# Kernel optimization log

Measured on AMD Instinct MI355X. Metric: run time of the kernel, lower is better.

## Reference

```python
import jax, jax.numpy as jnp
import numpy as np

B, N, C, H = 64, 1024, 512, 8
D = C // H            # head dim = 64
WIN = 32
M = 64                # num_landmarks
HP, WP = 8, 8         # closest_square_factors(64)
ITERS = 6
SCALE = D ** -0.5


def activ(x):
    # ExpLinearAfterThreshold with max_val=0: exp(clamp(x, max=0)) + relu(x)
    return jnp.exp(jnp.minimum(x, 0.0)) + jax.nn.relu(x)


def moore_penrose_iter_pinv(x, iters=ITERS):
    abs_x = jnp.abs(x)
    denom = jnp.max(abs_x.sum(axis=-1)) * jnp.max(abs_x.sum(axis=-2))
    z = jnp.swapaxes(x, -1, -2) / denom
    I = jnp.eye(x.shape[-1], dtype=x.dtype)
    for _ in range(iters):
        xz = x @ z
        z = 0.25 * z @ (13.0 * I - xz @ (15.0 * I - xz @ (7.0 * I - xz)))
    return z


def pool_landmarks(t):
    t = t.reshape(B, H, HP, WIN // HP, WP, WIN // WP, D)
    return t.mean(axis=(3, 5)).reshape(B, H, M, D)


def setup_inputs() -> dict:
    key = jax.random.key(0)
    ks = jax.random.split(key, 7)
    s = 0.02
    x = jax.random.normal(ks[0], (B, N, C), jnp.float32)
    Wq = jax.random.normal(ks[1], (C, C), jnp.float32) * s
    bq = jnp.zeros((C,), jnp.float32)
    Wkv = jax.random.normal(ks[2], (C, 2 * C), jnp.float32) * s
    bkv = jnp.zeros((2 * C,), jnp.float32)
    Wp = jax.random.normal(ks[3], (C, C), jnp.float32) * s
    bp = jnp.zeros((C,), jnp.float32)
    return {"x": x, "Wq": Wq, "bq": bq, "Wkv": Wkv, "bkv": bkv, "Wp": Wp, "bp": bp}


def reference(x, Wq, bq, Wkv, bkv, Wp, bp):
    Bsz = x.shape[0]
    q = (x @ Wq + bq).reshape(Bsz, N, H, D).transpose(0, 2, 1, 3) * SCALE  # [B,H,N,D]
    kv = (x @ Wkv + bkv).reshape(Bsz, N, 2, H, D).transpose(2, 0, 3, 1, 4)
    k, v = kv[0], kv[1]                                                    # [B,H,N,D]

    q_m = pool_landmarks(q)   # [B,H,M,D]
    k_m = pool_landmarks(k)   # [B,H,M,D]

    temp = activ(jnp.einsum('bhmd,bhnd->bhmn', q_m, k_m))   # [B,H,M,M]
    pinv = moore_penrose_iter_pinv(temp, ITERS)

    v1 = jnp.concatenate([v, jnp.ones_like(v[..., :1])], axis=-1)          # [B,H,N,D+1]
    kern_qkm = activ(jnp.einsum('bhnd,bhmd->bhnm', q, k_m))                # [B,H,N,M]
    kern_qmk_v = activ(jnp.einsum('bhmd,bhnd->bhmn', q_m, k)) @ v1         # [B,H,M,D+1]

    prod = kern_qkm @ (pinv @ kern_qmk_v)                                  # [B,H,N,D+1]
    out = prod[..., :-1] / (prod[..., -1:] + 1e-12)                        # [B,H,N,D]
    out = out.transpose(0, 2, 1, 3).reshape(Bsz, N, C)
    return out @ Wp + bp
```

## Files before the change

### kernel.cpp

```cpp
#include <hip/hip_runtime.h>

typedef _Float16 f16;
typedef _Float16 f16x4 __attribute__((ext_vector_type(4)));
typedef _Float16 f16x8 __attribute__((ext_vector_type(8)));
typedef float f32x4 __attribute__((ext_vector_type(4)));

#define MFMA16(a, b, c) __builtin_amdgcn_mfma_f32_16x16x32_f16((a), (b), (c), 0, 0, 0)

__device__ __forceinline__ void gload16(const void* g, void* l) {
  __builtin_amdgcn_global_load_lds(
      (const __attribute__((address_space(1))) void*)g,
      (__attribute__((address_space(3))) void*)l, 16, 0, 0);
}

__device__ __forceinline__ f16x8 lds8(const f16* buf, int row, int ch) {
  return *(const f16x8*)(buf + row * 64 + ((ch ^ (row & 7)) << 3));
}

#define VMW8 asm volatile("s_waitcnt vmcnt(8)" ::: "memory")
#define VMW0 asm volatile("s_waitcnt vmcnt(0)" ::: "memory")
#define BAR __builtin_amdgcn_s_barrier()


__global__ __launch_bounds__(256) void k_prep_w(
    const float* __restrict__ Wq, const float* __restrict__ Wkv,
    const float* __restrict__ Wp, const float* __restrict__ bq,
    const float* __restrict__ bkv, f16* __restrict__ WcT,
    f16* __restrict__ WpT, float* __restrict__ bc) {
  int b = blockIdx.x, t = threadIdx.x;
  if (b < 1536) {
    for (int kk = t; kk < 512; kk += 256) {
      float w = (b < 512) ? Wq[kk * 512 + b] : Wkv[kk * 1024 + (b - 512)];
      WcT[b * 512 + kk] = (f16)w;
    }
    if (t == 0) bc[b] = (b < 512) ? bq[b] : bkv[b - 512];
  } else {
    int pc = b - 1536;
    for (int kk = t; kk < 512; kk += 256)
      WpT[pc * 512 + kk] = (f16)Wp[kk * 512 + pc];
  }
}

__global__ __launch_bounds__(256) void k_prep_x(const float* __restrict__ x,
                                                f16* __restrict__ xh,
                                                float* __restrict__ xm) {
  __shared__ float pl[4][8][512];
  int bid = blockIdx.x;
  int b = bid >> 3, a = bid & 7;
  int tid = threadIdx.x;
  int tr = tid >> 6, cl = tid & 63;
  int c0 = cl * 8;
  float pacc[8][8];
#pragma unroll
  for (int i = 0; i < 8; i++)
#pragma unroll
    for (int j = 0; j < 8; j++) pacc[i][j] = 0.f;
#pragma unroll
  for (int j = 0; j < 32; j++) {
    int n = a * 128 + tr * 32 + j;
    const float* row = x + (size_t)(b * 1024 + n) * 512 + c0;
    float4 v0 = *(const float4*)row;
    float4 v1 = *(const float4*)(row + 4);
    f16x8 h;
    h[0] = (f16)v0.x; h[1] = (f16)v0.y; h[2] = (f16)v0.z; h[3] = (f16)v0.w;
    h[4] = (f16)v1.x; h[5] = (f16)v1.y; h[6] = (f16)v1.z; h[7] = (f16)v1.w;
    *(f16x8*)(xh + (size_t)(b * 1024 + n) * 512 + c0) = h;
    int cg = j >> 2;
    pacc[cg][0] += v0.x; pacc[cg][1] += v0.y; pacc[cg][2] += v0.z;
    pacc[cg][3] += v0.w; pacc[cg][4] += v1.x; pacc[cg][5] += v1.y;
    pacc[cg][6] += v1.z; pacc[cg][7] += v1.w;
  }
#pragma unroll
  for (int cg = 0; cg < 8; cg++) {
    *(float4*)&pl[tr][cg][c0] =
        make_float4(pacc[cg][0], pacc[cg][1], pacc[cg][2], pacc[cg][3]);
    *(float4*)&pl[tr][cg][c0 + 4] =
        make_float4(pacc[cg][4], pacc[cg][5], pacc[cg][6], pacc[cg][7]);
  }
  __syncthreads();
#pragma unroll
  for (int s = 0; s < 4; s++) {
    int o = tid + s * 256;
    int cg = o >> 7, c4 = (o & 127) << 2;
    float4 r0 = *(const float4*)&pl[0][cg][c4];
    float4 r1 = *(const float4*)&pl[1][cg][c4];
    float4 r2 = *(const float4*)&pl[2][cg][c4];
    float4 r3 = *(const float4*)&pl[3][cg][c4];
    float4 r;
    r.x = (r0.x + r1.x + r2.x + r3.x) * 0.0625f;
    r.y = (r0.y + r1.y + r2.y + r3.y) * 0.0625f;
    r.z = (r0.z + r1.z + r2.z + r3.z) * 0.0625f;
    r.w = (r0.w + r1.w + r2.w + r3.w) * 0.0625f;
    *(float4*)(xm + (size_t)(b * 64 + a * 8 + cg) * 512 + c4) = r;
  }
}

__global__ __launch_bounds__(512) void k_qkv(
    const f16* __restrict__ xh, const f16* __restrict__ WcT,
    const float* __restrict__ bc, f16* __restrict__ qb, f16* __restrict__ kb,
    f16* __restrict__ vb) {
  __shared__ f16 Al[2][256 * 64];
  __shared__ f16 Bl[2][256 * 64];
  int bid = blockIdx.x;
  int swz = (bid & 7) * 192 + (bid >> 3);
  int ct = swz % 6, rt = swz / 6;
  int m0 = rt * 256, n0 = ct * 256;
  int tid = threadIdx.x, lane = tid & 63, w = tid >> 6;
  int lr = lane & 15, hi = lane >> 4;
  int wr = w >> 2, wc = w & 3;

  int srow = tid >> 3;
  int cg = (tid & 7) ^ (srow & 7);
  const f16* gA = xh + (size_t)(m0 + srow) * 512 + cg * 8;
  const f16* gB = WcT + (size_t)(n0 + srow) * 512 + cg * 8;

  f32x4 acc[4][8] = {};

#define STG(BUF, K0)                                                \
  {                                                                 \
    _Pragma("unroll") for (int s = 0; s < 4; s++) {                 \
      gload16(gA + (K0) + s * 64 * 512, &Al[BUF][tid * 8 + s * 4096]); \
      gload16(gB + (K0) + s * 64 * 512, &Bl[BUF][tid * 8 + s * 4096]); \
    }                                                               \
  }
#define CMP(BUF)                                                    \
  {                                                                 \
    __builtin_amdgcn_s_setprio(1);                                  \
    _Pragma("unroll") for (int kc = 0; kc < 2; kc++) {              \
      f16x8 af[4], bf[8];                                           \
      _Pragma("unroll") for (int ni = 0; ni < 4; ni++)              \
          af[ni] = lds8(&Bl[BUF][0], wc * 64 + ni * 16 + lr, kc * 4 + hi); \
      _Pragma("unroll") for (int mi = 0; mi < 8; mi++)              \
          bf[mi] = lds8(&Al[BUF][0], wr * 128 + mi * 16 + lr, kc * 4 + hi); \
      _Pragma("unroll") for (int ni = 0; ni < 4; ni++)              \
          _Pragma("unroll") for (int mi = 0; mi < 8; mi++)          \
              acc[ni][mi] = MFMA16(af[ni], bf[mi], acc[ni][mi]);    \
    }                                                               \
    __builtin_amdgcn_s_setprio(0);                                  \
  }

  STG(0, 0);
  STG(1, 64);
  VMW8; BAR; CMP(0); BAR; STG(0, 2 * 64);
  VMW8; BAR; CMP(1); BAR; STG(1, 3 * 64);
  VMW8; BAR; CMP(0); BAR; STG(0, 4 * 64);
  VMW8; BAR; CMP(1); BAR; STG(1, 5 * 64);
  VMW8; BAR; CMP(0); BAR; STG(0, 6 * 64);
  VMW8; BAR; CMP(1); BAR; STG(1, 7 * 64);
  VMW8; BAR; CMP(0);
  VMW0; BAR; CMP(1);
#undef STG
#undef CMP

  int region = n0 >> 9;
  f16* dst = region == 0 ? qb : (region == 1 ? kb : vb);
  float scale = region == 0 ? 0.125f : 1.0f;
  int ncol0 = n0 - region * 512;
  float4 bias[4];
#pragma unroll
  for (int ni = 0; ni < 4; ni++)
    bias[ni] = *(const float4*)(bc + region * 512 + ncol0 + wc * 64 + ni * 16 +
                                hi * 4);
#pragma unroll
  for (int mi = 0; mi < 8; mi++) {
    int gr = m0 + wr * 128 + mi * 16 + lr;
    int b = gr >> 10, n = gr & 1023;
#pragma unroll
    for (int ni = 0; ni < 4; ni++) {
      int cc = ncol0 + wc * 64 + ni * 16 + hi * 4;
      int h = cc >> 6, d = cc & 63;
      f16x4 hv;
      hv[0] = (f16)((acc[ni][mi][0] + bias[ni].x) * scale);
      hv[1] = (f16)((acc[ni][mi][1] + bias[ni].y) * scale);
      hv[2] = (f16)((acc[ni][mi][2] + bias[ni].z) * scale);
      hv[3] = (f16)((acc[ni][mi][3] + bias[ni].w) * scale);
      *(f16x4*)(dst + (size_t)(((b * 8 + h) * 1024 + n) * 64 + d)) = hv;
    }
  }
}

__global__ __launch_bounds__(512) void k_qmkm(
    const float* __restrict__ xm, const float* __restrict__ Wq,
    const float* __restrict__ Wkv, const float* __restrict__ bq,
    const float* __restrict__ bkv, float* __restrict__ qm,
    float* __restrict__ km) {
  __shared__ float xl[16][512];
  int bid = blockIdx.x;
  int b = bid >> 2, mg = bid & 3;
  int tid = threadIdx.x;
  for (int s = 0; s < 4; s++) {
    int idx = (tid + s * 512) * 4;
    int r = idx >> 9, cc = idx & 511;
    *(float4*)&xl[r][cc] =
        *(const float4*)(xm + (b * 64 + mg * 16 + r) * 512 + cc);
  }
  __syncthreads();
  int oc = tid;
  float aq[16] = {}, ak[16] = {};
  for (int cc = 0; cc < 512; cc += 4) {
    float wq0 = Wq[(cc + 0) * 512 + oc], wq1 = Wq[(cc + 1) * 512 + oc];
    float wq2 = Wq[(cc + 2) * 512 + oc], wq3 = Wq[(cc + 3) * 512 + oc];
    float wk0 = Wkv[(cc + 0) * 1024 + oc], wk1 = Wkv[(cc + 1) * 1024 + oc];
    float wk2 = Wkv[(cc + 2) * 1024 + oc], wk3 = Wkv[(cc + 3) * 1024 + oc];
    for (int mi = 0; mi < 16; mi++) {
      float4 xv = *(const float4*)&xl[mi][cc];
      aq[mi] += xv.x * wq0 + xv.y * wq1 + xv.z * wq2 + xv.w * wq3;
      ak[mi] += xv.x * wk0 + xv.y * wk1 + xv.z * wk2 + xv.w * wk3;
    }
  }
  int h = oc >> 6, d = oc & 63;
  for (int mi = 0; mi < 16; mi++) {
    int m = mg * 16 + mi;
    int base = ((b * 8 + h) * 64 + m) * 64 + d;
    qm[base] = (aq[mi] + bq[oc]) * 0.125f;
    km[base] = ak[mi] + bkv[oc];
  }
}

__global__ __launch_bounds__(256) void k_temp(const float* __restrict__ qm,
                                              const float* __restrict__ km,
                                              float* __restrict__ temp,
                                              unsigned* __restrict__ den) {
  __shared__ float ql[64][68], kl[64][68];
  __shared__ float rs[64], cs[64];
  int g = blockIdx.x, tid = threadIdx.x;
  for (int idx = tid; idx < 4096; idx += 256) {
    int r = idx >> 6, c = idx & 63;
    ql[r][c] = qm[g * 4096 + idx];
    kl[r][c] = km[g * 4096 + idx];
  }
  __syncthreads();
  int ti = tid >> 4, tj = tid & 15;
  float acc[4][4] = {};
  for (int kk = 0; kk < 64; kk += 4) {
    float4 qa[4], kb[4];
    for (int i = 0; i < 4; i++) qa[i] = *(const float4*)&ql[ti * 4 + i][kk];
    for (int j = 0; j < 4; j++) kb[j] = *(const float4*)&kl[tj * 4 + j][kk];
    for (int i = 0; i < 4; i++)
      for (int j = 0; j < 4; j++)
        acc[i][j] += qa[i].x * kb[j].x + qa[i].y * kb[j].y +
                     qa[i].z * kb[j].z + qa[i].w * kb[j].w;
  }
  float e[4][4];
  for (int i = 0; i < 4; i++)
    for (int j = 0; j < 4; j++) {
      float xx = acc[i][j];
      e[i][j] = xx > 0.f ? 1.f + xx : __expf(xx);
    }
  __syncthreads();
  for (int i = 0; i < 4; i++)
    for (int j = 0; j < 4; j++) kl[ti * 4 + i][tj * 4 + j] = e[i][j];
  __syncthreads();
  for (int idx = tid; idx < 4096; idx += 256)
    temp[g * 4096 + idx] = kl[idx >> 6][idx & 63];
  if (tid < 64) {
    float s = 0.f;
    for (int j = 0; j < 64; j++) s += kl[tid][j];
    rs[tid] = s;
  } else if (tid < 128) {
    int c = tid - 64;
    float s = 0.f;
    for (int i = 0; i < 64; i++) s += kl[i][c];
    cs[c] = s;
  }
  __syncthreads();
  if (tid == 0) {
    float mx = rs[0];
    for (int i = 1; i < 64; i++) mx = fmaxf(mx, rs[i]);
    atomicMax(den + 0, __float_as_uint(mx));
  }
  if (tid == 1) {
    float mx = cs[0];
    for (int i = 1; i < 64; i++) mx = fmaxf(mx, cs[i]);
    atomicMax(den + 1, __float_as_uint(mx));
  }
}

__global__ __launch_bounds__(256) void k_pinv(const float* __restrict__ temp,
                                              const unsigned* __restrict__ den,
                                              float* __restrict__ z) {
  __shared__ f16 wh[64][72], Zh[64][72], ZhT[64][72], GhT[64][72], W1h[64][72],
      W2h[64][72];
  __shared__ float colZ[64];
  int g = blockIdx.x, tid = threadIdx.x;
  float dn = __uint_as_float(den[0]) * __uint_as_float(den[1]);
  float inv = 1.0f / dn;
  for (int idx = tid; idx < 4096; idx += 256) {
    int r = idx >> 6, c = idx & 63;
    float t = temp[g * 4096 + idx];
    wh[r][c] = (f16)(t - 1.0f);
    ZhT[r][c] = (f16)(t * inv);
  }
  __syncthreads();
  for (int idx = tid; idx < 4096; idx += 256) {
    int r = idx >> 6, c = idx & 63;
    Zh[r][c] = ZhT[c][r];
  }
  __syncthreads();
  int lane = tid & 63, w = tid >> 6, lr = lane & 15, hi = lane >> 4;
  int rb = w * 16;
  for (int it = 0; it < 6; it++) {
    if (tid < 64) {
      float s = 0.f;
      for (int i = 0; i < 64; i++) s += (float)ZhT[tid][i];
      colZ[tid] = s;
    }
    __syncthreads();
    {
      f32x4 acc[4] = {};
      for (int kc = 0; kc < 2; kc++) {
        f16x8 a = *(const f16x8*)&wh[rb + lr][kc * 32 + hi * 8];
        for (int cj = 0; cj < 4; cj++)
          acc[cj] = MFMA16(
              a, *(const f16x8*)&ZhT[cj * 16 + lr][kc * 32 + hi * 8], acc[cj]);
      }
      for (int cj = 0; cj < 4; cj++)
        for (int rg = 0; rg < 4; rg++) {
          int rr = rb + hi * 4 + rg, cc = cj * 16 + lr;
          GhT[cc][rr] = (f16)(acc[cj][rg] + colZ[cc]);
        }
    }
    __syncthreads();
    {
      f32x4 acc[4] = {};
      for (int kc = 0; kc < 2; kc++) {
        f16x8 a = *(const f16x8*)&Zh[rb + lr][kc * 32 + hi * 8];
        for (int cj = 0; cj < 4; cj++)
          acc[cj] = MFMA16(
              a, *(const f16x8*)&GhT[cj * 16 + lr][kc * 32 + hi * 8], acc[cj]);
      }
      for (int cj = 0; cj < 4; cj++)
        for (int rg = 0; rg < 4; rg++)
          W1h[rb + hi * 4 + rg][cj * 16 + lr] = (f16)acc[cj][rg];
    }
    __syncthreads();
    {
      f32x4 acc[4] = {};
      for (int kc = 0; kc < 2; kc++) {
        f16x8 a = *(const f16x8*)&W1h[rb + lr][kc * 32 + hi * 8];
        for (int cj = 0; cj < 4; cj++)
          acc[cj] = MFMA16(
              a, *(const f16x8*)&GhT[cj * 16 + lr][kc * 32 + hi * 8], acc[cj]);
      }
      for (int cj = 0; cj < 4; cj++)
        for (int rg = 0; rg < 4; rg++)
          W2h[rb + hi * 4 + rg][cj * 16 + lr] = (f16)acc[cj][rg];
    }
    __syncthreads();
    {
      f32x4 acc[4] = {};
      for (int kc = 0; kc < 2; kc++) {
        f16x8 a = *(const f16x8*)&W2h[rb + lr][kc * 32 + hi * 8];
        for (int cj = 0; cj < 4; cj++)
          acc[cj] = MFMA16(
              a, *(const f16x8*)&GhT[cj * 16 + lr][kc * 32 + hi * 8], acc[cj]);
      }
      for (int cj = 0; cj < 4; cj++)
        for (int rg = 0; rg < 4; rg++) {
          int rr = rb + hi * 4 + rg, cc = cj * 16 + lr;
          float zn = 3.25f * (float)Zh[rr][cc] - 3.75f * (float)W1h[rr][cc] +
                     1.75f * (float)W2h[rr][cc] - 0.25f * acc[cj][rg];
          if (it == 5) {
            z[g * 4096 + rr * 64 + cc] = zn;
          } else {
            Zh[rr][cc] = (f16)zn;
            ZhT[cc][rr] = (f16)zn;
          }
        }
    }
    __syncthreads();
  }
}

__global__ __launch_bounds__(256) void k_kqmkv(const float* __restrict__ qm,
                                               const f16* __restrict__ kb,
                                               const f16* __restrict__ vb,
                                               float* __restrict__ kq) {
  __shared__ f16 qh[64][72];
  __shared__ f16 Sl[64][136];
  __shared__ f16 vt[80][136];
  int g = blockIdx.x, tid = threadIdx.x;
  int lane = tid & 63, w = tid >> 6, lr = lane & 15, hi = lane >> 4;
  for (int idx = tid; idx < 4096; idx += 256) {
    int r = idx >> 6, c = idx & 63;
    qh[r][c] = (f16)qm[g * 4096 + idx];
  }
  for (int idx = tid; idx < 16 * 136; idx += 256) {
    int r = 64 + idx / 136, c = idx % 136;
    vt[r][c] = (r == 64) ? (f16)1.0f : (f16)0.0f;
  }
  f32x4 acc2[5] = {};
  const f16* kbase = kb + g * 65536;
  const f16* vbase = vb + g * 65536;
  for (int n0 = 0; n0 < 1024; n0 += 128) {
    __syncthreads();
    for (int s = 0; s < 4; s++) {
      int cid = tid + s * 256;
      int r = cid >> 3, ch = cid & 7;
      f16x8 v8 = *(const f16x8*)(vbase + (n0 + r) * 64 + ch * 8);
      for (int j = 0; j < 8; j++) vt[ch * 8 + j][r] = v8[j];
    }
    __syncthreads();
    f32x4 sacc[8] = {};
    for (int kc = 0; kc < 2; kc++) {
      f16x8 a = *(const f16x8*)&qh[w * 16 + lr][kc * 32 + hi * 8];
      for (int cj = 0; cj < 8; cj++) {
        f16x8 bv =
            *(const f16x8*)(kbase + (n0 + cj * 16 + lr) * 64 + kc * 32 + hi * 8);
        sacc[cj] = MFMA16(a, bv, sacc[cj]);
      }
    }
    for (int cj = 0; cj < 8; cj++)
      for (int rg = 0; rg < 4; rg++) {
        float xx = sacc[cj][rg];
        float e = xx > 0.f ? 1.f + xx : __expf(xx);
        Sl[w * 16 + hi * 4 + rg][cj * 16 + lr] = (f16)e;
      }
    __syncthreads();
    for (int kc2 = 0; kc2 < 4; kc2++) {
      f16x8 a = *(const f16x8*)&Sl[w * 16 + lr][kc2 * 32 + hi * 8];
      for (int ce = 0; ce < 5; ce++)
        acc2[ce] = MFMA16(
            a, *(const f16x8*)&vt[ce * 16 + lr][kc2 * 32 + hi * 8], acc2[ce]);
    }
  }
  for (int ce = 0; ce < 5; ce++)
    for (int rg = 0; rg < 4; rg++)
      kq[g * 5120 + (w * 16 + hi * 4 + rg) * 80 + ce * 16 + lr] = acc2[ce][rg];
}

__global__ __launch_bounds__(256) void k_w2(const float* __restrict__ z,
                                            const float* __restrict__ kq,
                                            f16* __restrict__ w2t) {
  __shared__ float zl[64][68];
  __shared__ float kl[64][84];
  int g = blockIdx.x, tid = threadIdx.x;
  for (int idx = tid; idx < 4096; idx += 256)
    zl[idx >> 6][idx & 63] = z[g * 4096 + idx];
  for (int idx = tid; idx < 5120; idx += 256)
    kl[idx / 80][idx % 80] = kq[g * 5120 + idx];
  __syncthreads();
  int ti = tid >> 4, tj = tid & 15;
  float acc[4][5] = {};
  for (int kk = 0; kk < 64; kk++) {
    float a0 = zl[ti * 4 + 0][kk], a1 = zl[ti * 4 + 1][kk];
    float a2 = zl[ti * 4 + 2][kk], a3 = zl[ti * 4 + 3][kk];
    for (int j = 0; j < 5; j++) {
      float bv = kl[kk][tj * 5 + j];
      acc[0][j] += a0 * bv; acc[1][j] += a1 * bv;
      acc[2][j] += a2 * bv; acc[3][j] += a3 * bv;
    }
  }
  for (int i = 0; i < 4; i++)
    for (int j = 0; j < 5; j++)
      w2t[g * 5120 + (tj * 5 + j) * 64 + (ti * 4 + i)] = (f16)acc[i][j];
}

__global__ __launch_bounds__(256) void k_attn(const f16* __restrict__ qb,
                                              const float* __restrict__ km,
                                              const f16* __restrict__ w2t,
                                              f16* __restrict__ attn) {
  __shared__ f16 kmh[64][72];
  __shared__ f16 w2l[80][72];
  __shared__ f16 Sl[128][72];
  int g = blockIdx.x;
  int b = g >> 3, h = g & 7;
  int tid = threadIdx.x, lane = tid & 63, w = tid >> 6, lr = lane & 15,
      hi = lane >> 4;
  for (int idx = tid; idx < 4096; idx += 256)
    kmh[idx >> 6][idx & 63] = (f16)km[g * 4096 + idx];
  for (int idx = tid; idx < 5120; idx += 256)
    w2l[idx >> 6][idx & 63] = w2t[g * 5120 + idx];
  __syncthreads();
  for (int nt = 0; nt < 8; nt++) {
    int n0 = nt * 128;
    if (nt) __syncthreads();
    const f16* qbase = qb + g * 65536 + n0 * 64;
    f32x4 sacc[2][4] = {};
    for (int kc = 0; kc < 2; kc++)
      for (int ri = 0; ri < 2; ri++) {
        f16x8 a = *(const f16x8*)(qbase + (w * 32 + ri * 16 + lr) * 64 +
                                  kc * 32 + hi * 8);
        for (int cj = 0; cj < 4; cj++)
          sacc[ri][cj] = MFMA16(
              a, *(const f16x8*)&kmh[cj * 16 + lr][kc * 32 + hi * 8],
              sacc[ri][cj]);
      }
    for (int ri = 0; ri < 2; ri++)
      for (int cj = 0; cj < 4; cj++)
        for (int rg = 0; rg < 4; rg++) {
          float xx = sacc[ri][cj][rg];
          Sl[w * 32 + ri * 16 + hi * 4 + rg][cj * 16 + lr] =
              (f16)(xx > 0.f ? 1.f + xx : __expf(xx));
        }
    __syncthreads();
    f32x4 accP[5][2] = {};
    for (int kc = 0; kc < 2; kc++)
      for (int ri = 0; ri < 2; ri++) {
        f16x8 bfrag =
            *(const f16x8*)&Sl[w * 32 + ri * 16 + lr][kc * 32 + hi * 8];
        for (int ce = 0; ce < 5; ce++)
          accP[ce][ri] = MFMA16(
              *(const f16x8*)&w2l[ce * 16 + lr][kc * 32 + hi * 8], bfrag,
              accP[ce][ri]);
      }
    for (int ri = 0; ri < 2; ri++) {
      float dv = __shfl(accP[4][ri][0], lr, 64);
      float rd = 1.0f / (dv + 1e-12f);
      int n = w * 32 + ri * 16 + lr;
      for (int ce = 0; ce < 4; ce++) {
        f16x4 hv;
        hv[0] = (f16)(accP[ce][ri][0] * rd);
        hv[1] = (f16)(accP[ce][ri][1] * rd);
        hv[2] = (f16)(accP[ce][ri][2] * rd);
        hv[3] = (f16)(accP[ce][ri][3] * rd);
        *(f16x4*)(attn + (size_t)(b * 1024 + n0 + n) * 512 + h * 64 +
                  ce * 16 + hi * 4) = hv;
      }
    }
  }
}

__global__ __launch_bounds__(512) void k_out(const f16* __restrict__ ah,
                                             const f16* __restrict__ WpT,
                                             const float* __restrict__ bp,
                                             float* __restrict__ out) {
  __shared__ f16 Al[2][256 * 64];
  __shared__ f16 Bl[2][256 * 64];
  int bid = blockIdx.x;
  int swz = (bid & 7) * 64 + (bid >> 3);
  int ct = swz & 1, rt = swz >> 1;
  int m0 = rt * 256, n0 = ct * 256;
  int tid = threadIdx.x, lane = tid & 63, w = tid >> 6;
  int lr = lane & 15, hi = lane >> 4;
  int wr = w >> 2, wc = w & 3;

  int srow = tid >> 3;
  int cg = (tid & 7) ^ (srow & 7);
  const f16* gA = ah + (size_t)(m0 + srow) * 512 + cg * 8;
  const f16* gB = WpT + (size_t)(n0 + srow) * 512 + cg * 8;

  f32x4 acc[4][8] = {};

#define STG(BUF, K0)                                                \
  {                                                                 \
    _Pragma("unroll") for (int s = 0; s < 4; s++) {                 \
      gload16(gA + (K0) + s * 64 * 512, &Al[BUF][tid * 8 + s * 4096]); \
      gload16(gB + (K0) + s * 64 * 512, &Bl[BUF][tid * 8 + s * 4096]); \
    }                                                               \
  }
#define CMP(BUF)                                                    \
  {                                                                 \
    __builtin_amdgcn_s_setprio(1);                                  \
    _Pragma("unroll") for (int kc = 0; kc < 2; kc++) {              \
      f16x8 af[4], bf[8];                                           \
      _Pragma("unroll") for (int ni = 0; ni < 4; ni++)              \
          af[ni] = lds8(&Bl[BUF][0], wc * 64 + ni * 16 + lr, kc * 4 + hi); \
      _Pragma("unroll") for (int mi = 0; mi < 8; mi++)              \
          bf[mi] = lds8(&Al[BUF][0], wr * 128 + mi * 16 + lr, kc * 4 + hi); \
      _Pragma("unroll") for (int ni = 0; ni < 4; ni++)              \
          _Pragma("unroll") for (int mi = 0; mi < 8; mi++)          \
              acc[ni][mi] = MFMA16(af[ni], bf[mi], acc[ni][mi]);    \
    }                                                               \
    __builtin_amdgcn_s_setprio(0);                                  \
  }

  STG(0, 0);
  STG(1, 64);
  VMW8; BAR; CMP(0); BAR; STG(0, 2 * 64);
  VMW8; BAR; CMP(1); BAR; STG(1, 3 * 64);
  VMW8; BAR; CMP(0); BAR; STG(0, 4 * 64);
  VMW8; BAR; CMP(1); BAR; STG(1, 5 * 64);
  VMW8; BAR; CMP(0); BAR; STG(0, 6 * 64);
  VMW8; BAR; CMP(1); BAR; STG(1, 7 * 64);
  VMW8; BAR; CMP(0);
  VMW0; BAR; CMP(1);
#undef STG
#undef CMP

  float4 bias[4];
#pragma unroll
  for (int ni = 0; ni < 4; ni++)
    bias[ni] = *(const float4*)(bp + n0 + wc * 64 + ni * 16 + hi * 4);
#pragma unroll
  for (int mi = 0; mi < 8; mi++) {
    int gr = m0 + wr * 128 + mi * 16 + lr;
#pragma unroll
    for (int ni = 0; ni < 4; ni++) {
      int gc = n0 + wc * 64 + ni * 16 + hi * 4;
      float4 v;
      v.x = acc[ni][mi][0] + bias[ni].x;
      v.y = acc[ni][mi][1] + bias[ni].y;
      v.z = acc[ni][mi][2] + bias[ni].z;
      v.w = acc[ni][mi][3] + bias[ni].w;
      *(float4*)(out + (size_t)gr * 512 + gc) = v;
    }
  }
}

extern "C" void kernel_launch(void* const* d_in, const int* in_sizes, int n_in,
                              void* d_out, int out_size, void* d_ws,
                              size_t ws_size, hipStream_t stream) {
  (void)in_sizes; (void)n_in; (void)out_size; (void)ws_size;
  const float* x = (const float*)d_in[0];
  const float* Wq = (const float*)d_in[1];
  const float* bq = (const float*)d_in[2];
  const float* Wkv = (const float*)d_in[3];
  const float* bkv = (const float*)d_in[4];
  const float* Wp = (const float*)d_in[5];
  const float* bp = (const float*)d_in[6];
  float* outp = (float*)d_out;

  char* ws = (char*)d_ws;
  size_t o = 0;
  auto take = [&](size_t bytes) {
    char* p = ws + o;
    o += (bytes + 255) & ~(size_t)255;
    return p;
  };
  f16* WcT = (f16*)take(1536 * 512 * 2);
  f16* WpT = (f16*)take(512 * 512 * 2);
  float* bc = (float*)take(1536 * 4);
  f16* xh = (f16*)take(67108864);
  f16* qb = (f16*)take(67108864);
  f16* kb = (f16*)take(67108864);
  f16* vb = (f16*)take(67108864);

  char* od = (char*)d_out;
  size_t s = 0;
  auto sub = [&](size_t bytes) {
    char* p = od + s;
    s += (bytes + 255) & ~(size_t)255;
    return p;
  };
  float* xm = (float*)sub(64 * 64 * 512 * 4);
  float* qm = (float*)sub(512 * 4096 * 4);
  float* km = (float*)sub(512 * 4096 * 4);
  float* temp = (float*)sub(512 * 4096 * 4);
  float* zz = (float*)sub(512 * 4096 * 4);
  float* kq = (float*)sub(512 * 64 * 80 * 4);
  f16* w2t = (f16*)sub(512 * 80 * 64 * 2);
  unsigned* den = (unsigned*)sub(256);
  f16* attn = vb;

  hipLaunchKernelGGL(k_prep_w, dim3(2048), dim3(256), 0, stream, Wq, Wkv, Wp,
                     bq, bkv, WcT, WpT, bc);
  hipLaunchKernelGGL(k_prep_x, dim3(512), dim3(256), 0, stream, x, xh, xm);
  hipLaunchKernelGGL(k_qkv, dim3(1536), dim3(512), 0, stream, xh, WcT, bc,
                     qb, kb, vb);
  hipLaunchKernelGGL(k_qmkm, dim3(256), dim3(512), 0, stream, xm, Wq, Wkv, bq,
                     bkv, qm, km);
  hipMemsetAsync(den, 0, 8, stream);
  hipLaunchKernelGGL(k_temp, dim3(512), dim3(256), 0, stream, qm, km, temp,
                     den);
  hipLaunchKernelGGL(k_pinv, dim3(512), dim3(256), 0, stream, temp, den, zz);
  hipLaunchKernelGGL(k_kqmkv, dim3(512), dim3(256), 0, stream, qm, kb, vb, kq);
  hipLaunchKernelGGL(k_w2, dim3(512), dim3(256), 0, stream, zz, kq, w2t);
  hipLaunchKernelGGL(k_attn, dim3(512), dim3(256), 0, stream, qb, km, w2t,
                     attn);
  hipLaunchKernelGGL(k_out, dim3(512), dim3(512), 0, stream, attn, WpT, bp,
                     outp);
}
```

Baseline: 572.0 us.

## Interleave global-to-LDS prefetch with MFMA phases in QKV and projection GEMMs

Replaces the coarse double-buffered stage/compute loop in both large GEMM kernels with a finer schedule. Each K-tile is split into four phases, and each phase issues two prefetch loads for the next tile before its MFMAs run. Fragments are loaded per phase, and barriers plus a scheduling fence separate LDS reads from the MFMA block. The aim is to hide global load latency behind compute and spread out memory issue, at the cost of more barriers per tile and tighter wait counts.

```diff
diff --git a/kernel.cpp b/kernel.cpp
--- a/kernel.cpp
+++ b/kernel.cpp
@@ -17,8 +17,9 @@
   return *(const f16x8*)(buf + row * 64 + ((ch ^ (row & 7)) << 3));
 }
 
-#define VMW8 asm volatile("s_waitcnt vmcnt(8)" ::: "memory")
 #define VMW0 asm volatile("s_waitcnt vmcnt(0)" ::: "memory")
+#define VMW2 asm volatile("s_waitcnt vmcnt(2)" ::: "memory")
+#define VMW4 asm volatile("s_waitcnt vmcnt(4)" ::: "memory")
 #define BAR __builtin_amdgcn_s_barrier()
 
 
@@ -95,6 +96,40 @@
   }
 }
 
+#define SA(BUF, K0, S) gload16(gA + (K0) + (S)*64*512, &Al[BUF][tid*8 + (S)*4096]);
+#define SB(BUF, K0, S) gload16(gB + (K0) + (S)*64*512, &Bl[BUF][tid*8 + (S)*4096]);
+#define PHASE(P, Q, ...)                                                  \
+  {                                                                       \
+    f16x8 af[4], bf[4];                                                   \
+    _Pragma("unroll") for (int ni = 0; ni < 4; ni++)                      \
+      af[ni] = lds8(&Bl[P][0], wc*64 + ni*16 + lr, ((Q)&1)*4 + hi);       \
+    _Pragma("unroll") for (int mj = 0; mj < 4; mj++)                      \
+      bf[mj] = lds8(&Al[P][0], wr*128 + (((Q)>>1)*4+mj)*16 + lr, ((Q)&1)*4 + hi); \
+    __VA_ARGS__                                                           \
+    BAR;                                                                  \
+    asm volatile("s_waitcnt lgkmcnt(0)" ::: "memory");                    \
+    __builtin_amdgcn_sched_barrier(0);                                    \
+    __builtin_amdgcn_s_setprio(1);                                        \
+    _Pragma("unroll") for (int ni = 0; ni < 4; ni++)                      \
+      _Pragma("unroll") for (int mj = 0; mj < 4; mj++)                    \
+        acc[ni][((Q)>>1)*4+mj] = MFMA16(af[ni], bf[mj], acc[ni][((Q)>>1)*4+mj]); \
+    __builtin_amdgcn_s_setprio(0);                                        \
+    BAR;                                                                  \
+  }
+#define GROUP(T)                                                          \
+  VMW2; BAR;                                                              \
+  PHASE((T)&1, 0, SB(1-((T)&1), ((T)+1)*64, 0) SB(1-((T)&1), ((T)+1)*64, 1)) \
+  PHASE((T)&1, 1, SB(1-((T)&1), ((T)+1)*64, 2) SB(1-((T)&1), ((T)+1)*64, 3)) \
+  VMW4; BAR;                                                              \
+  PHASE((T)&1, 2, SA(1-((T)&1), ((T)+1)*64, 0) SA(1-((T)&1), ((T)+1)*64, 2)) \
+  PHASE((T)&1, 3, SA(1-((T)&1), ((T)+1)*64, 1) SA(1-((T)&1), ((T)+1)*64, 3))
+#define GROUP_LAST(T)                                                     \
+  VMW0; BAR;                                                              \
+  PHASE((T)&1, 0, ) PHASE((T)&1, 1, ) PHASE((T)&1, 2, ) PHASE((T)&1, 3, )
+#define PROLOGUE                                                          \
+  SB(0, 0, 0) SB(0, 0, 1) SB(0, 0, 2) SB(0, 0, 3)                         \
+  SA(0, 0, 0) SA(0, 0, 2) SA(0, 0, 1) SA(0, 0, 3)
+
 __global__ __launch_bounds__(512) void k_qkv(
     const f16* __restrict__ xh, const f16* __restrict__ WcT,
     const float* __restrict__ bc, f16* __restrict__ qb, f16* __restrict__ kb,
@@ -116,41 +151,9 @@
 
   f32x4 acc[4][8] = {};
 
-#define STG(BUF, K0)                                                \
-  {                                                                 \
-    _Pragma("unroll") for (int s = 0; s < 4; s++) {                 \
-      gload16(gA + (K0) + s * 64 * 512, &Al[BUF][tid * 8 + s * 4096]); \
-      gload16(gB + (K0) + s * 64 * 512, &Bl[BUF][tid * 8 + s * 4096]); \
-    }                                                               \
-  }
-#define CMP(BUF)                                                    \
-  {                                                                 \
-    __builtin_amdgcn_s_setprio(1);                                  \
-    _Pragma("unroll") for (int kc = 0; kc < 2; kc++) {              \
-      f16x8 af[4], bf[8];                                           \
-      _Pragma("unroll") for (int ni = 0; ni < 4; ni++)              \
-          af[ni] = lds8(&Bl[BUF][0], wc * 64 + ni * 16 + lr, kc * 4 + hi); \
-      _Pragma("unroll") for (int mi = 0; mi < 8; mi++)              \
-          bf[mi] = lds8(&Al[BUF][0], wr * 128 + mi * 16 + lr, kc * 4 + hi); \
-      _Pragma("unroll") for (int ni = 0; ni < 4; ni++)              \
-          _Pragma("unroll") for (int mi = 0; mi < 8; mi++)          \
-              acc[ni][mi] = MFMA16(af[ni], bf[mi], acc[ni][mi]);    \
-    }                                                               \
-    __builtin_amdgcn_s_setprio(0);                                  \
-  }
-
-  STG(0, 0);
-  STG(1, 64);
-  VMW8; BAR; CMP(0); BAR; STG(0, 2 * 64);
-  VMW8; BAR; CMP(1); BAR; STG(1, 3 * 64);
-  VMW8; BAR; CMP(0); BAR; STG(0, 4 * 64);
-  VMW8; BAR; CMP(1); BAR; STG(1, 5 * 64);
-  VMW8; BAR; CMP(0); BAR; STG(0, 6 * 64);
-  VMW8; BAR; CMP(1); BAR; STG(1, 7 * 64);
-  VMW8; BAR; CMP(0);
-  VMW0; BAR; CMP(1);
-#undef STG
-#undef CMP
+  PROLOGUE
+  GROUP(0) GROUP(1) GROUP(2) GROUP(3) GROUP(4) GROUP(5) GROUP(6)
+  GROUP_LAST(7)
 
   int region = n0 >> 9;
   f16* dst = region == 0 ? qb : (region == 1 ? kb : vb);
@@ -542,41 +545,9 @@
 
   f32x4 acc[4][8] = {};
 
-#define STG(BUF, K0)                                                \
-  {                                                                 \
-    _Pragma("unroll") for (int s = 0; s < 4; s++) {                 \
-      gload16(gA + (K0) + s * 64 * 512, &Al[BUF][tid * 8 + s * 4096]); \
-      gload16(gB + (K0) + s * 64 * 512, &Bl[BUF][tid * 8 + s * 4096]); \
-    }                                                               \
-  }
-#define CMP(BUF)                                                    \
-  {                                                                 \
-    __builtin_amdgcn_s_setprio(1);                                  \
-    _Pragma("unroll") for (int kc = 0; kc < 2; kc++) {              \
-      f16x8 af[4], bf[8];                                           \
-      _Pragma("unroll") for (int ni = 0; ni < 4; ni++)              \
-          af[ni] = lds8(&Bl[BUF][0], wc * 64 + ni * 16 + lr, kc * 4 + hi); \
-      _Pragma("unroll") for (int mi = 0; mi < 8; mi++)              \
-          bf[mi] = lds8(&Al[BUF][0], wr * 128 + mi * 16 + lr, kc * 4 + hi); \
-      _Pragma("unroll") for (int ni = 0; ni < 4; ni++)              \
-          _Pragma("unroll") for (int mi = 0; mi < 8; mi++)          \
-              acc[ni][mi] = MFMA16(af[ni], bf[mi], acc[ni][mi]);    \
-    }                                                               \
-    __builtin_amdgcn_s_setprio(0);                                  \
-  }
-
-  STG(0, 0);
-  STG(1, 64);
-  VMW8; BAR; CMP(0); BAR; STG(0, 2 * 64);
-  VMW8; BAR; CMP(1); BAR; STG(1, 3 * 64);
-  VMW8; BAR; CMP(0); BAR; STG(0, 4 * 64);
-  VMW8; BAR; CMP(1); BAR; STG(1, 5 * 64);
-  VMW8; BAR; CMP(0); BAR; STG(0, 6 * 64);
-  VMW8; BAR; CMP(1); BAR; STG(1, 7 * 64);
-  VMW8; BAR; CMP(0);
-  VMW0; BAR; CMP(1);
-#undef STG
-#undef CMP
+  PROLOGUE
+  GROUP(0) GROUP(1) GROUP(2) GROUP(3) GROUP(4) GROUP(5) GROUP(6)
+  GROUP_LAST(7)
 
   float4 bias[4];
 #pragma unroll
```

Measured after the change: 593.7 us. 1.04x slower.

## Merge prep kernels, fold memset, shrink GEMM tiles to 128x128 with 256 threads

Applied to the files above, without the earlier changes.

Combines the weight-prep and x-prep kernels into one launch and zeroes the denominator counters inside it, so the separate memset and one kernel launch go away. The QKV and output-projection GEMMs move from 256x256 tiles with 512 threads to 128x128 tiles with 256 threads. This quadruples the block count and halves LDS use per block, which is meant to improve occupancy and load balance across CUs. The cost is lower per-block data reuse and more global and L2 traffic for the operand tiles.

```diff
diff --git a/kernel.cpp b/kernel.cpp
--- a/kernel.cpp
+++ b/kernel.cpp
@@ -22,32 +22,33 @@
 #define BAR __builtin_amdgcn_s_barrier()
 
 
-__global__ __launch_bounds__(256) void k_prep_w(
-    const float* __restrict__ Wq, const float* __restrict__ Wkv,
-    const float* __restrict__ Wp, const float* __restrict__ bq,
-    const float* __restrict__ bkv, f16* __restrict__ WcT,
-    f16* __restrict__ WpT, float* __restrict__ bc) {
-  int b = blockIdx.x, t = threadIdx.x;
-  if (b < 1536) {
-    for (int kk = t; kk < 512; kk += 256) {
-      float w = (b < 512) ? Wq[kk * 512 + b] : Wkv[kk * 1024 + (b - 512)];
-      WcT[b * 512 + kk] = (f16)w;
-    }
-    if (t == 0) bc[b] = (b < 512) ? bq[b] : bkv[b - 512];
-  } else {
-    int pc = b - 1536;
-    for (int kk = t; kk < 512; kk += 256)
-      WpT[pc * 512 + kk] = (f16)Wp[kk * 512 + pc];
-  }
-}
-
-__global__ __launch_bounds__(256) void k_prep_x(const float* __restrict__ x,
-                                                f16* __restrict__ xh,
-                                                float* __restrict__ xm) {
+__global__ __launch_bounds__(256) void k_prep(
+    const float* __restrict__ x, const float* __restrict__ Wq,
+    const float* __restrict__ Wkv, const float* __restrict__ Wp,
+    const float* __restrict__ bq, const float* __restrict__ bkv,
+    f16* __restrict__ xh, float* __restrict__ xm, f16* __restrict__ WcT,
+    f16* __restrict__ WpT, float* __restrict__ bc,
+    unsigned* __restrict__ den) {
   __shared__ float pl[4][8][512];
   int bid = blockIdx.x;
+  int tid = threadIdx.x;
+  if (bid >= 512) {
+    int b = bid - 512;
+    if (b < 1536) {
+      for (int kk = tid; kk < 512; kk += 256) {
+        float w = (b < 512) ? Wq[kk * 512 + b] : Wkv[kk * 1024 + (b - 512)];
+        WcT[b * 512 + kk] = (f16)w;
+      }
+      if (tid == 0) bc[b] = (b < 512) ? bq[b] : bkv[b - 512];
+      if (b == 0 && tid == 1) { den[0] = 0u; den[1] = 0u; }
+    } else {
+      int pc = b - 1536;
+      for (int kk = tid; kk < 512; kk += 256)
+        WpT[pc * 512 + kk] = (f16)Wp[kk * 512 + pc];
+    }
+    return;
+  }
   int b = bid >> 3, a = bid & 7;
-  int tid = threadIdx.x;
   int tr = tid >> 6, cl = tid & 63;
   int c0 = cl * 8;
   float pacc[8][8];
@@ -95,45 +96,45 @@
   }
 }
 
-__global__ __launch_bounds__(512) void k_qkv(
+__global__ __launch_bounds__(256) void k_qkv(
     const f16* __restrict__ xh, const f16* __restrict__ WcT,
     const float* __restrict__ bc, f16* __restrict__ qb, f16* __restrict__ kb,
     f16* __restrict__ vb) {
-  __shared__ f16 Al[2][256 * 64];
-  __shared__ f16 Bl[2][256 * 64];
+  __shared__ f16 Al[2][128 * 64];
+  __shared__ f16 Bl[2][128 * 64];
   int bid = blockIdx.x;
-  int swz = (bid & 7) * 192 + (bid >> 3);
-  int ct = swz % 6, rt = swz / 6;
-  int m0 = rt * 256, n0 = ct * 256;
+  int swz = (bid & 7) * 768 + (bid >> 3);
+  int ct = swz % 12, rt = swz / 12;
+  int m0 = rt * 128, n0 = ct * 128;
   int tid = threadIdx.x, lane = tid & 63, w = tid >> 6;
   int lr = lane & 15, hi = lane >> 4;
-  int wr = w >> 2, wc = w & 3;
+  int wr = w >> 1, wc = w & 1;
 
   int srow = tid >> 3;
   int cg = (tid & 7) ^ (srow & 7);
   const f16* gA = xh + (size_t)(m0 + srow) * 512 + cg * 8;
   const f16* gB = WcT + (size_t)(n0 + srow) * 512 + cg * 8;
 
-  f32x4 acc[4][8] = {};
+  f32x4 acc[4][4] = {};
 
 #define STG(BUF, K0)                                                \
   {                                                                 \
     _Pragma("unroll") for (int s = 0; s < 4; s++) {                 \
-      gload16(gA + (K0) + s * 64 * 512, &Al[BUF][tid * 8 + s * 4096]); \
-      gload16(gB + (K0) + s * 64 * 512, &Bl[BUF][tid * 8 + s * 4096]); \
+      gload16(gA + (K0) + s * 32 * 512, &Al[BUF][tid * 8 + s * 2048]); \
+      gload16(gB + (K0) + s * 32 * 512, &Bl[BUF][tid * 8 + s * 2048]); \
     }                                                               \
   }
 #define CMP(BUF)                                                    \
   {                                                                 \
     __builtin_amdgcn_s_setprio(1);                                  \
     _Pragma("unroll") for (int kc = 0; kc < 2; kc++) {              \
-      f16x8 af[4], bf[8];                                           \
+      f16x8 af[4], bf[4];                                           \
       _Pragma("unroll") for (int ni = 0; ni < 4; ni++)              \
           af[ni] = lds8(&Bl[BUF][0], wc * 64 + ni * 16 + lr, kc * 4 + hi); \
-      _Pragma("unroll") for (int mi = 0; mi < 8; mi++)              \
-          bf[mi] = lds8(&Al[BUF][0], wr * 128 + mi * 16 + lr, kc * 4 + hi); \
+      _Pragma("unroll") for (int mi = 0; mi < 4; mi++)              \
+          bf[mi] = lds8(&Al[BUF][0], wr * 64 + mi * 16 + lr, kc * 4 + hi); \
       _Pragma("unroll") for (int ni = 0; ni < 4; ni++)              \
-          _Pragma("unroll") for (int mi = 0; mi < 8; mi++)          \
+          _Pragma("unroll") for (int mi = 0; mi < 4; mi++)          \
               acc[ni][mi] = MFMA16(af[ni], bf[mi], acc[ni][mi]);    \
     }                                                               \
     __builtin_amdgcn_s_setprio(0);                                  \
@@ -162,8 +163,8 @@
     bias[ni] = *(const float4*)(bc + region * 512 + ncol0 + wc * 64 + ni * 16 +
                                 hi * 4);
 #pragma unroll
-  for (int mi = 0; mi < 8; mi++) {
-    int gr = m0 + wr * 128 + mi * 16 + lr;
+  for (int mi = 0; mi < 4; mi++) {
+    int gr = m0 + wr * 64 + mi * 16 + lr;
     int b = gr >> 10, n = gr & 1023;
 #pragma unroll
     for (int ni = 0; ni < 4; ni++) {
@@ -521,45 +522,45 @@
   }
 }
 
-__global__ __launch_bounds__(512) void k_out(const f16* __restrict__ ah,
+__global__ __launch_bounds__(256) void k_out(const f16* __restrict__ ah,
                                              const f16* __restrict__ WpT,
                                              const float* __restrict__ bp,
                                              float* __restrict__ out) {
-  __shared__ f16 Al[2][256 * 64];
-  __shared__ f16 Bl[2][256 * 64];
+  __shared__ f16 Al[2][128 * 64];
+  __shared__ f16 Bl[2][128 * 64];
   int bid = blockIdx.x;
-  int swz = (bid & 7) * 64 + (bid >> 3);
-  int ct = swz & 1, rt = swz >> 1;
-  int m0 = rt * 256, n0 = ct * 256;
+  int swz = (bid & 7) * 256 + (bid >> 3);
+  int ct = swz & 3, rt = swz >> 2;
+  int m0 = rt * 128, n0 = ct * 128;
   int tid = threadIdx.x, lane = tid & 63, w = tid >> 6;
   int lr = lane & 15, hi = lane >> 4;
-  int wr = w >> 2, wc = w & 3;
+  int wr = w >> 1, wc = w & 1;
 
   int srow = tid >> 3;
   int cg = (tid & 7) ^ (srow & 7);
   const f16* gA = ah + (size_t)(m0 + srow) * 512 + cg * 8;
   const f16* gB = WpT + (size_t)(n0 + srow) * 512 + cg * 8;
 
-  f32x4 acc[4][8] = {};
+  f32x4 acc[4][4] = {};
 
 #define STG(BUF, K0)                                                \
   {                                                                 \
     _Pragma("unroll") for (int s = 0; s < 4; s++) {                 \
-      gload16(gA + (K0) + s * 64 * 512, &Al[BUF][tid * 8 + s * 4096]); \
-      gload16(gB + (K0) + s * 64 * 512, &Bl[BUF][tid * 8 + s * 4096]); \
+      gload16(gA + (K0) + s * 32 * 512, &Al[BUF][tid * 8 + s * 2048]); \
+      gload16(gB + (K0) + s * 32 * 512, &Bl[BUF][tid * 8 + s * 2048]); \
     }                                                               \
   }
 #define CMP(BUF)                                                    \
   {                                                                 \
     __builtin_amdgcn_s_setprio(1);                                  \
     _Pragma("unroll") for (int kc = 0; kc < 2; kc++) {              \
-      f16x8 af[4], bf[8];                                           \
+      f16x8 af[4], bf[4];                                           \
       _Pragma("unroll") for (int ni = 0; ni < 4; ni++)              \
           af[ni] = lds8(&Bl[BUF][0], wc * 64 + ni * 16 + lr, kc * 4 + hi); \
-      _Pragma("unroll") for (int mi = 0; mi < 8; mi++)              \
-          bf[mi] = lds8(&Al[BUF][0], wr * 128 + mi * 16 + lr, kc * 4 + hi); \
+      _Pragma("unroll") for (int mi = 0; mi < 4; mi++)              \
+          bf[mi] = lds8(&Al[BUF][0], wr * 64 + mi * 16 + lr, kc * 4 + hi); \
       _Pragma("unroll") for (int ni = 0; ni < 4; ni++)              \
-          _Pragma("unroll") for (int mi = 0; mi < 8; mi++)          \
+          _Pragma("unroll") for (int mi = 0; mi < 4; mi++)          \
               acc[ni][mi] = MFMA16(af[ni], bf[mi], acc[ni][mi]);    \
     }                                                               \
     __builtin_amdgcn_s_setprio(0);                                  \
@@ -583,8 +584,8 @@
   for (int ni = 0; ni < 4; ni++)
     bias[ni] = *(const float4*)(bp + n0 + wc * 64 + ni * 16 + hi * 4);
 #pragma unroll
-  for (int mi = 0; mi < 8; mi++) {
-    int gr = m0 + wr * 128 + mi * 16 + lr;
+  for (int mi = 0; mi < 4; mi++) {
+    int gr = m0 + wr * 64 + mi * 16 + lr;
 #pragma unroll
     for (int ni = 0; ni < 4; ni++) {
       int gc = n0 + wc * 64 + ni * 16 + hi * 4;
@@ -643,14 +644,12 @@
   unsigned* den = (unsigned*)sub(256);
   f16* attn = vb;
 
-  hipLaunchKernelGGL(k_prep_w, dim3(2048), dim3(256), 0, stream, Wq, Wkv, Wp,
-                     bq, bkv, WcT, WpT, bc);
-  hipLaunchKernelGGL(k_prep_x, dim3(512), dim3(256), 0, stream, x, xh, xm);
-  hipLaunchKernelGGL(k_qkv, dim3(1536), dim3(512), 0, stream, xh, WcT, bc,
+  hipLaunchKernelGGL(k_prep, dim3(2560), dim3(256), 0, stream, x, Wq, Wkv, Wp,
+                     bq, bkv, xh, xm, WcT, WpT, bc, den);
+  hipLaunchKernelGGL(k_qkv, dim3(6144), dim3(256), 0, stream, xh, WcT, bc,
                      qb, kb, vb);
   hipLaunchKernelGGL(k_qmkm, dim3(256), dim3(512), 0, stream, xm, Wq, Wkv, bq,
                      bkv, qm, km);
-  hipMemsetAsync(den, 0, 8, stream);
   hipLaunchKernelGGL(k_temp, dim3(512), dim3(256), 0, stream, qm, km, temp,
                      den);
   hipLaunchKernelGGL(k_pinv, dim3(512), dim3(256), 0, stream, temp, den, zz);
@@ -658,6 +657,6 @@
   hipLaunchKernelGGL(k_w2, dim3(512), dim3(256), 0, stream, zz, kq, w2t);
   hipLaunchKernelGGL(k_attn, dim3(512), dim3(256), 0, stream, qb, km, w2t,
                      attn);
-  hipLaunchKernelGGL(k_out, dim3(512), dim3(512), 0, stream, attn, WpT, bp,
+  hipLaunchKernelGGL(k_out, dim3(2048), dim3(256), 0, stream, attn, WpT, bp,
                      outp);
 }
```

After: 593.3 us. +3.7%, slower.

## Fuse kqmkv, w2 and attn kernels; merge prep kernels and memset

Applied to the files above, without the earlier changes.

Merges the weight-prep and x-prep kernels into one launch, which also zeroes the denominator counters so the separate memset goes away. Fuses the kernel_qmk·v, pinv·kq product and the attention kernel into a single per-(batch, head) kernel. The fused kernel keeps kq and w2 in reused shared memory instead of round-tripping them through global buffers. This cuts launch count and intermediate global traffic, but the fused kernel uses a larger shared footprint (~59KB), which may lower occupancy.

```diff
diff --git a/kernel.cpp b/kernel.cpp
--- a/kernel.cpp
+++ b/kernel.cpp
@@ -22,32 +22,33 @@
 #define BAR __builtin_amdgcn_s_barrier()
 
 
-__global__ __launch_bounds__(256) void k_prep_w(
-    const float* __restrict__ Wq, const float* __restrict__ Wkv,
-    const float* __restrict__ Wp, const float* __restrict__ bq,
-    const float* __restrict__ bkv, f16* __restrict__ WcT,
-    f16* __restrict__ WpT, float* __restrict__ bc) {
-  int b = blockIdx.x, t = threadIdx.x;
-  if (b < 1536) {
-    for (int kk = t; kk < 512; kk += 256) {
-      float w = (b < 512) ? Wq[kk * 512 + b] : Wkv[kk * 1024 + (b - 512)];
-      WcT[b * 512 + kk] = (f16)w;
-    }
-    if (t == 0) bc[b] = (b < 512) ? bq[b] : bkv[b - 512];
-  } else {
-    int pc = b - 1536;
-    for (int kk = t; kk < 512; kk += 256)
-      WpT[pc * 512 + kk] = (f16)Wp[kk * 512 + pc];
-  }
-}
-
-__global__ __launch_bounds__(256) void k_prep_x(const float* __restrict__ x,
-                                                f16* __restrict__ xh,
-                                                float* __restrict__ xm) {
+__global__ __launch_bounds__(256) void k_prep(
+    const float* __restrict__ x, const float* __restrict__ Wq,
+    const float* __restrict__ Wkv, const float* __restrict__ Wp,
+    const float* __restrict__ bq, const float* __restrict__ bkv,
+    f16* __restrict__ xh, float* __restrict__ xm, f16* __restrict__ WcT,
+    f16* __restrict__ WpT, float* __restrict__ bc,
+    unsigned* __restrict__ den) {
   __shared__ float pl[4][8][512];
   int bid = blockIdx.x;
+  int tid = threadIdx.x;
+  if (bid >= 512) {
+    int b = bid - 512;
+    if (b < 1536) {
+      for (int kk = tid; kk < 512; kk += 256) {
+        float w = (b < 512) ? Wq[kk * 512 + b] : Wkv[kk * 1024 + (b - 512)];
+        WcT[b * 512 + kk] = (f16)w;
+      }
+      if (tid == 0) bc[b] = (b < 512) ? bq[b] : bkv[b - 512];
+      if (b == 0 && tid == 1) { den[0] = 0u; den[1] = 0u; }
+    } else {
+      int pc = b - 1536;
+      for (int kk = tid; kk < 512; kk += 256)
+        WpT[pc * 512 + kk] = (f16)Wp[kk * 512 + pc];
+    }
+    return;
+  }
   int b = bid >> 3, a = bid & 7;
-  int tid = threadIdx.x;
   int tr = tid >> 6, cl = tid & 63;
   int c0 = cl * 8;
   float pacc[8][8];
@@ -372,15 +373,18 @@
   }
 }
 
-__global__ __launch_bounds__(256) void k_kqmkv(const float* __restrict__ qm,
-                                               const f16* __restrict__ kb,
-                                               const f16* __restrict__ vb,
-                                               float* __restrict__ kq) {
-  __shared__ f16 qh[64][72];
-  __shared__ f16 Sl[64][136];
-  __shared__ f16 vt[80][136];
+__global__ __launch_bounds__(256) void k_kwa(
+    const float* __restrict__ qm, const f16* __restrict__ kb,
+    const f16* __restrict__ vb, const float* __restrict__ zz,
+    const float* __restrict__ km, const f16* __restrict__ qb,
+    f16* __restrict__ attn) {
+  __shared__ __align__(16) char smem[59904];
   int g = blockIdx.x, tid = threadIdx.x;
   int lane = tid & 63, w = tid >> 6, lr = lane & 15, hi = lane >> 4;
+  f16(*qh)[72] = (f16(*)[72])smem;
+  f16(*vt)[136] = (f16(*)[136])(smem + 9216);
+  f16(*Slk)[136] = (f16(*)[136])(smem + 30976);
+  f16(*w2l)[72] = (f16(*)[72])(smem + 48384);
   for (int idx = tid; idx < 4096; idx += 256) {
     int r = idx >> 6, c = idx & 63;
     qh[r][c] = (f16)qm[g * 4096 + idx];
@@ -413,64 +417,48 @@
     for (int cj = 0; cj < 8; cj++)
       for (int rg = 0; rg < 4; rg++) {
         float xx = sacc[cj][rg];
-        float e = xx > 0.f ? 1.f + xx : __expf(xx);
-        Sl[w * 16 + hi * 4 + rg][cj * 16 + lr] = (f16)e;
+        Slk[w * 16 + hi * 4 + rg][cj * 16 + lr] =
+            (f16)(xx > 0.f ? 1.f + xx : __expf(xx));
       }
     __syncthreads();
     for (int kc2 = 0; kc2 < 4; kc2++) {
-      f16x8 a = *(const f16x8*)&Sl[w * 16 + lr][kc2 * 32 + hi * 8];
+      f16x8 a = *(const f16x8*)&Slk[w * 16 + lr][kc2 * 32 + hi * 8];
       for (int ce = 0; ce < 5; ce++)
         acc2[ce] = MFMA16(
             a, *(const f16x8*)&vt[ce * 16 + lr][kc2 * 32 + hi * 8], acc2[ce]);
     }
   }
+  __syncthreads();
+  float(*kql)[84] = (float(*)[84])smem;
+  float(*zl)[68] = (float(*)[68])(smem + 30976);
   for (int ce = 0; ce < 5; ce++)
     for (int rg = 0; rg < 4; rg++)
-      kq[g * 5120 + (w * 16 + hi * 4 + rg) * 80 + ce * 16 + lr] = acc2[ce][rg];
-}
-
-__global__ __launch_bounds__(256) void k_w2(const float* __restrict__ z,
-                                            const float* __restrict__ kq,
-                                            f16* __restrict__ w2t) {
-  __shared__ float zl[64][68];
-  __shared__ float kl[64][84];
-  int g = blockIdx.x, tid = threadIdx.x;
+      kql[w * 16 + hi * 4 + rg][ce * 16 + lr] = acc2[ce][rg];
   for (int idx = tid; idx < 4096; idx += 256)
-    zl[idx >> 6][idx & 63] = z[g * 4096 + idx];
-  for (int idx = tid; idx < 5120; idx += 256)
-    kl[idx / 80][idx % 80] = kq[g * 5120 + idx];
-  __syncthreads();
-  int ti = tid >> 4, tj = tid & 15;
-  float acc[4][5] = {};
-  for (int kk = 0; kk < 64; kk++) {
-    float a0 = zl[ti * 4 + 0][kk], a1 = zl[ti * 4 + 1][kk];
-    float a2 = zl[ti * 4 + 2][kk], a3 = zl[ti * 4 + 3][kk];
-    for (int j = 0; j < 5; j++) {
-      float bv = kl[kk][tj * 5 + j];
-      acc[0][j] += a0 * bv; acc[1][j] += a1 * bv;
-      acc[2][j] += a2 * bv; acc[3][j] += a3 * bv;
-    }
-  }
-  for (int i = 0; i < 4; i++)
-    for (int j = 0; j < 5; j++)
-      w2t[g * 5120 + (tj * 5 + j) * 64 + (ti * 4 + i)] = (f16)acc[i][j];
-}
-
-__global__ __launch_bounds__(256) void k_attn(const f16* __restrict__ qb,
-                                              const float* __restrict__ km,
-                                              const f16* __restrict__ w2t,
-                                              f16* __restrict__ attn) {
-  __shared__ f16 kmh[64][72];
-  __shared__ f16 w2l[80][72];
-  __shared__ f16 Sl[128][72];
-  int g = blockIdx.x;
+    zl[idx >> 6][idx & 63] = zz[g * 4096 + idx];
+  __syncthreads();
+  {
+    int ti = tid >> 4, tj = tid & 15;
+    float acc[4][5] = {};
+    for (int kk = 0; kk < 64; kk++) {
+      float a0 = zl[ti * 4 + 0][kk], a1 = zl[ti * 4 + 1][kk];
+      float a2 = zl[ti * 4 + 2][kk], a3 = zl[ti * 4 + 3][kk];
+      for (int j = 0; j < 5; j++) {
+        float bv = kql[kk][tj * 5 + j];
+        acc[0][j] += a0 * bv; acc[1][j] += a1 * bv;
+        acc[2][j] += a2 * bv; acc[3][j] += a3 * bv;
+      }
+    }
+    for (int i = 0; i < 4; i++)
+      for (int j = 0; j < 5; j++)
+        w2l[tj * 5 + j][ti * 4 + i] = (f16)acc[i][j];
+  }
+  __syncthreads();
+  f16(*kmh)[72] = (f16(*)[72])smem;
+  f16(*Sl)[72] = (f16(*)[72])(smem + 9216);
   int b = g >> 3, h = g & 7;
-  int tid = threadIdx.x, lane = tid & 63, w = tid >> 6, lr = lane & 15,
-      hi = lane >> 4;
   for (int idx = tid; idx < 4096; idx += 256)
     kmh[idx >> 6][idx & 63] = (f16)km[g * 4096 + idx];
-  for (int idx = tid; idx < 5120; idx += 256)
-    w2l[idx >> 6][idx & 63] = w2t[g * 5120 + idx];
   __syncthreads();
   for (int nt = 0; nt < 8; nt++) {
     int n0 = nt * 128;
@@ -638,26 +626,20 @@
   float* km = (float*)sub(512 * 4096 * 4);
   float* temp = (float*)sub(512 * 4096 * 4);
   float* zz = (float*)sub(512 * 4096 * 4);
-  float* kq = (float*)sub(512 * 64 * 80 * 4);
-  f16* w2t = (f16*)sub(512 * 80 * 64 * 2);
   unsigned* den = (unsigned*)sub(256);
-  f16* attn = vb;
-
-  hipLaunchKernelGGL(k_prep_w, dim3(2048), dim3(256), 0, stream, Wq, Wkv, Wp,
-                     bq, bkv, WcT, WpT, bc);
-  hipLaunchKernelGGL(k_prep_x, dim3(512), dim3(256), 0, stream, x, xh, xm);
+  f16* attn = xh;
+
+  hipLaunchKernelGGL(k_prep, dim3(2560), dim3(256), 0, stream, x, Wq, Wkv, Wp,
+                     bq, bkv, xh, xm, WcT, WpT, bc, den);
   hipLaunchKernelGGL(k_qkv, dim3(1536), dim3(512), 0, stream, xh, WcT, bc,
                      qb, kb, vb);
   hipLaunchKernelGGL(k_qmkm, dim3(256), dim3(512), 0, stream, xm, Wq, Wkv, bq,
                      bkv, qm, km);
-  hipMemsetAsync(den, 0, 8, stream);
   hipLaunchKernelGGL(k_temp, dim3(512), dim3(256), 0, stream, qm, km, temp,
                      den);
   hipLaunchKernelGGL(k_pinv, dim3(512), dim3(256), 0, stream, temp, den, zz);
-  hipLaunchKernelGGL(k_kqmkv, dim3(512), dim3(256), 0, stream, qm, kb, vb, kq);
-  hipLaunchKernelGGL(k_w2, dim3(512), dim3(256), 0, stream, zz, kq, w2t);
-  hipLaunchKernelGGL(k_attn, dim3(512), dim3(256), 0, stream, qb, km, w2t,
-                     attn);
+  hipLaunchKernelGGL(k_kwa, dim3(512), dim3(256), 0, stream, qm, kb, vb, zz,
+                     km, qb, attn);
   hipLaunchKernelGGL(k_out, dim3(512), dim3(512), 0, stream, attn, WpT, bp,
                      outp);
 }
```

After: 499.2 us. 1.15x faster.
